# Kernel optimization log

Hardware: AMD Instinct MI355X
Metric: run time of the kernel (lower is better)

## Reference

```python
import jax, jax.numpy as jnp
import numpy as np


def setup_inputs() -> dict:
    key = jax.random.key(0)
    k1, k2, k3 = jax.random.split(key, 3)
    S, G, B, C, P = 3, 8, 2048, 512, 64
    node_feats = jax.random.normal(k1, (S, G * B, C), dtype=jnp.float32)
    weight = jax.random.normal(k2, (P, C), dtype=jnp.float32)
    smooth_factor = jax.random.normal(k3, (P,), dtype=jnp.float32)
    return {
        "node_feats": node_feats,
        "weight": weight,
        "smooth_factor": smooth_factor,
        "batch_size": B,
        "num_graphs": G,
    }


def reference(node_feats, weight, smooth_factor, batch_size, num_graphs):
    # node_feats: [S, N_scale, C] (scales stacked; torch version takes a list and cats)
    S, Ns, C = node_feats.shape
    P = weight.shape[0]
    x = node_feats.reshape(-1, C)                       # [N, C], N = S*Ns

    # RBF-style score: (2*c.x - |x|^2 - |c|^2), clamped at 0, scaled by beta
    cx = x @ weight.T                                   # [N, P]
    x_sq = jnp.sum(x * x, axis=1, keepdims=True)        # [N, 1]
    c_sq = jnp.sum(weight * weight, axis=1)[None, :]    # [1, P]
    beta = jax.nn.sigmoid(smooth_factor)                # [P]
    logits = jnp.minimum(2.0 * cx - x_sq - c_sq, 0.0) / beta[None, :]
    assign = jax.nn.softmax(logits, axis=1)             # [N, P]

    # Per-graph weighted sum (uniform batch_list), accumulated across scales:
    # out[g] = sum_{s,n in graph g} assign[s,g,n]^T feats[s,g,n]
    a = assign.reshape(S, num_graphs, batch_size, P)
    f = node_feats.reshape(S, num_graphs, batch_size, C)
    outputs = jnp.einsum('sgnp,sgnc->gpc', a, f)        # [G, P, C]
    return outputs, assign
```

## Files before the change

kernel.cpp:

```cpp
#include <hip/hip_runtime.h>
#include <math.h>

#define S_ 3
#define G_ 8
#define B_ 2048
#define C_ 512
#define P_ 64
#define N_ (S_ * G_ * B_)

typedef __attribute__((ext_vector_type(8))) short short8;
typedef __attribute__((ext_vector_type(4))) float f32x4;
typedef __attribute__((ext_vector_type(4))) unsigned int uint4v;
typedef __attribute__((ext_vector_type(2))) unsigned int uint2v;

__device__ __forceinline__ unsigned f2bf1(float f) {
    union { float f; unsigned u; } c; c.f = f;
    unsigned u = c.u;
    u += 0x7fffu + ((u >> 16) & 1u);
    return u >> 16;
}
__device__ __forceinline__ unsigned pk2(float a, float b) {
    return f2bf1(a) | (f2bf1(b) << 16);
}

__global__ void zero_kernel(float* __restrict__ out) {
    int i = blockIdx.x * blockDim.x + threadIdx.x;
    ((f32x4*)out)[i] = (f32x4){0.f, 0.f, 0.f, 0.f};
}

__global__ __launch_bounds__(64) void prep_kernel(
    const float* __restrict__ w, const float* __restrict__ sf,
    unsigned short* __restrict__ wb, float* __restrict__ csq,
    float* __restrict__ rbeta)
{
    const int p = blockIdx.x, l = threadIdx.x;
    const float* wr = w + (size_t)p * C_ + l * 8;
    f32x4 a = *(const f32x4*)wr;
    f32x4 b = *(const f32x4*)(wr + 4);
    float s = a[0]*a[0] + a[1]*a[1] + a[2]*a[2] + a[3]*a[3]
            + b[0]*b[0] + b[1]*b[1] + b[2]*b[2] + b[3]*b[3];
    uint4v pk;
    pk.x = pk2(a[0], a[1]); pk.y = pk2(a[2], a[3]);
    pk.z = pk2(b[0], b[1]); pk.w = pk2(b[2], b[3]);
    *(uint4v*)&wb[(size_t)p * C_ + l * 8] = pk;
#pragma unroll
    for (int off = 1; off < 64; off <<= 1) s += __shfl_xor(s, off, 64);
    if (l == 0) csq[p] = s;
    if (p == 0) rbeta[l] = 1.0f + expf(-sf[l]);
}

__global__ __launch_bounds__(256) void assign_v2(
    const float* __restrict__ x, const unsigned short* __restrict__ wb,
    const float* __restrict__ csq, const float* __restrict__ rbeta,
    float* __restrict__ assign, unsigned short* __restrict__ a_t)
{
    __shared__ float lg[64 * 68];

    const int t    = threadIdx.x;
    const int lane = t & 63;
    const int wv   = t >> 6;
    const int q    = lane >> 4;
    const int col  = lane & 15;
    const int n0   = blockIdx.x * 64;
    const int myrow = 16 * wv + col;

    const float* xr = x + (size_t)(n0 + myrow) * C_ + q * 8;

    float csqv[4], rbv[4];
#pragma unroll
    for (int t4 = 0; t4 < 4; ++t4) {
        csqv[t4] = csq[16 * t4 + col];
        rbv[t4]  = rbeta[16 * t4 + col];
    }

    f32x4 acc[4];
#pragma unroll
    for (int i = 0; i < 4; ++i) acc[i] = (f32x4){0.f, 0.f, 0.f, 0.f};
    float xsq = 0.f;

#pragma unroll
    for (int ks = 0; ks < 16; ++ks) {
        f32x4 a = *(const f32x4*)(xr + ks * 32);
        f32x4 b = *(const f32x4*)(xr + ks * 32 + 4);
        xsq += a[0]*a[0] + a[1]*a[1] + a[2]*a[2] + a[3]*a[3]
             + b[0]*b[0] + b[1]*b[1] + b[2]*b[2] + b[3]*b[3];
        union { uint4v u; short8 s; } cvt;
        cvt.u.x = pk2(a[0], a[1]); cvt.u.y = pk2(a[2], a[3]);
        cvt.u.z = pk2(b[0], b[1]); cvt.u.w = pk2(b[2], b[3]);
        short8 af = cvt.s;
#pragma unroll
        for (int t4 = 0; t4 < 4; ++t4) {
            short8 bf = *(const short8*)&wb[(size_t)(16 * t4 + col) * C_ + ks * 32 + q * 8];
            acc[t4] = __builtin_amdgcn_mfma_f32_16x16x32_bf16(af, bf, acc[t4], 0, 0, 0);
        }
    }

    xsq += __shfl_xor(xsq, 16, 64);
    xsq += __shfl_xor(xsq, 32, 64);
    float xsqr[4];
#pragma unroll
    for (int reg = 0; reg < 4; ++reg) xsqr[reg] = __shfl(xsq, 4 * q + reg, 64);

#pragma unroll
    for (int reg = 0; reg < 4; ++reg) {
        const int row = 16 * wv + 4 * q + reg;
        float vv[4], vmax = -3.4e38f;
#pragma unroll
        for (int t4 = 0; t4 < 4; ++t4) {
            float v = 2.0f * acc[t4][reg] - xsqr[reg] - csqv[t4];
            v = fminf(v, 0.0f) * rbv[t4];
            vv[t4] = v;
            vmax = fmaxf(vmax, v);
        }
#pragma unroll
        for (int off = 1; off < 16; off <<= 1)
            vmax = fmaxf(vmax, __shfl_xor(vmax, off, 64));
        float e[4], ss = 0.f;
#pragma unroll
        for (int t4 = 0; t4 < 4; ++t4) { e[t4] = __expf(vv[t4] - vmax); ss += e[t4]; }
#pragma unroll
        for (int off = 1; off < 16; off <<= 1)
            ss += __shfl_xor(ss, off, 64);
        const float inv = 1.0f / ss;
#pragma unroll
        for (int t4 = 0; t4 < 4; ++t4) {
            const float val = e[t4] * inv;
            assign[(size_t)(n0 + row) * P_ + 16 * t4 + col] = val;
            lg[row * 68 + 16 * t4 + col] = val;
        }
    }
    __syncthreads();

    const int p  = t >> 2;
    const int nq = t & 3;
    float v[16];
#pragma unroll
    for (int i = 0; i < 16; ++i) v[i] = lg[(nq * 16 + i) * 68 + p];
    uint4v d0, d1;
    d0.x = pk2(v[0], v[1]);  d0.y = pk2(v[2], v[3]);
    d0.z = pk2(v[4], v[5]);  d0.w = pk2(v[6], v[7]);
    d1.x = pk2(v[8], v[9]);  d1.y = pk2(v[10], v[11]);
    d1.z = pk2(v[12], v[13]); d1.w = pk2(v[14], v[15]);
    unsigned short* dst = a_t + (size_t)p * N_ + n0 + nq * 16;
    *(uint4v*)dst = d0;
    *(uint4v*)(dst + 8) = d1;
}

__global__ __launch_bounds__(256) void group_v3(
    const float* __restrict__ x, const unsigned short* __restrict__ a_t,
    float* __restrict__ out)
{
    __shared__ unsigned int fsu[64 * 36];

    const int t    = threadIdx.x;
    const int lane = t & 63;
    const int wv   = t >> 6;
    const int q    = lane >> 4;
    const int col  = lane & 15;
    const int g    = blockIdx.x;
    const int c0   = blockIdx.y * 64;
    const int kc   = blockIdx.z;
    const int sc   = kc >> 2;
    const int b0   = (kc & 3) * 512;
    const int srow = t >> 4;
    const int scol = t & 15;

    const size_t base = (size_t)sc * (G_ * B_) + (size_t)g * B_ + b0;
    const unsigned short* at_row = a_t + (size_t)(16 * wv + col) * N_ + base;

    f32x4 acc[4];
#pragma unroll
    for (int i = 0; i < 4; ++i) acc[i] = (f32x4){0.f, 0.f, 0.f, 0.f};

    for (int ch = 0; ch < 8; ++ch) {
        const int nb = ch * 64;
        const size_t rbase = (base + nb + srow * 4) * C_ + c0 + scol * 4;
        f32x4 m0 = *(const f32x4*)(x + rbase);
        f32x4 m1 = *(const f32x4*)(x + rbase + C_);
        f32x4 m2 = *(const f32x4*)(x + rbase + 2 * C_);
        f32x4 m3 = *(const f32x4*)(x + rbase + 3 * C_);
        const int sw_w = (scol & 6) << 3;
        const int nsw  = (srow * 4) ^ sw_w;
#pragma unroll
        for (int cc = 0; cc < 4; ++cc) {
            uint2v u;
            u.x = pk2(m0[cc], m1[cc]);
            u.y = pk2(m2[cc], m3[cc]);
            const int cl = scol * 4 + cc;
            *(uint2v*)&fsu[cl * 36 + (nsw >> 1)] = u;
        }
        __syncthreads();

#pragma unroll
        for (int stp = 0; stp < 2; ++stp) {
            const int kb = stp * 32 + q * 8;
            short8 af = *(const short8*)(at_row + nb + kb);
#pragma unroll
            for (int t4 = 0; t4 < 4; ++t4) {
                const int c  = 16 * t4 + col;
                const int sw = ((c >> 2) & 6) << 3;
                short8 bf = *(const short8*)&fsu[c * 36 + ((kb ^ sw) >> 1)];
                acc[t4] = __builtin_amdgcn_mfma_f32_16x16x32_bf16(af, bf, acc[t4], 0, 0, 0);
            }
        }
        __syncthreads();
    }

#pragma unroll
    for (int t4 = 0; t4 < 4; ++t4) {
#pragma unroll
        for (int reg = 0; reg < 4; ++reg) {
            const int p = 16 * wv + 4 * q + reg;
            const int c = c0 + 16 * t4 + col;
            atomicAdd(&out[(size_t)g * (P_ * C_) + (size_t)p * C_ + c], acc[t4][reg]);
        }
    }
}

extern "C" void kernel_launch(void* const* d_in, const int* in_sizes, int n_in,
                              void* d_out, int out_size, void* d_ws, size_t ws_size,
                              hipStream_t stream) {
    const float* x  = (const float*)d_in[0];
    const float* w  = (const float*)d_in[1];
    const float* sf = (const float*)d_in[2];

    float* out    = (float*)d_out;
    float* assign = out + (size_t)G_ * P_ * C_;

    unsigned short* wb    = (unsigned short*)d_ws;
    float*          csq   = (float*)((char*)d_ws + 65536);
    float*          rbeta = (float*)((char*)d_ws + 65792);
    unsigned short* a_t   = (unsigned short*)((char*)d_ws + 66048);

    zero_kernel<<<(G_ * P_ * C_) / (4 * 256), 256, 0, stream>>>(out);
    prep_kernel<<<P_, 64, 0, stream>>>(w, sf, wb, csq, rbeta);
    assign_v2<<<N_ / 64, 256, 0, stream>>>(x, wb, csq, rbeta, assign, a_t);
    dim3 gridB(G_, C_ / 64, 12);
    group_v3<<<gridB, 256, 0, stream>>>(x, a_t, out);
}
```

Measured before the change: 194.3 us.

## Stage x and weight tiles through LDS in assign and group GEMM kernels

The assign kernel now handles 128 rows per block and stages coalesced 64-column x chunks and bf16 weight chunks in shared memory. Each wave reuses the shared weight fragments across two M-tiles instead of re-reading them from global memory per lane. The group kernel now stages assignment rows in LDS as well and re-partitions the MFMA tiles so each wave owns a C slice. The intent is better coalescing and reuse of global loads, at the cost of more LDS traffic, extra barriers and fewer blocks in the assign kernel.

```diff
diff --git a/kernel.cpp b/kernel.cpp
--- a/kernel.cpp
+++ b/kernel.cpp
@@ -49,108 +49,158 @@
     if (p == 0) rbeta[l] = 1.0f + expf(-sf[l]);
 }
 
-__global__ __launch_bounds__(256) void assign_v2(
+#define XS_STR 68
+#define WS_STR 72
+__global__ __launch_bounds__(256, 3) void assign_gemm(
     const float* __restrict__ x, const unsigned short* __restrict__ wb,
     const float* __restrict__ csq, const float* __restrict__ rbeta,
     float* __restrict__ assign, unsigned short* __restrict__ a_t)
 {
-    __shared__ float lg[64 * 68];
+    __shared__ __align__(16) char smem[128 * XS_STR * 4 + 64 * WS_STR * 2];
+    float* xs = (float*)smem;
+    unsigned short* wsh = (unsigned short*)(smem + 128 * XS_STR * 4);
+    float* lg = (float*)smem;
 
     const int t    = threadIdx.x;
     const int lane = t & 63;
     const int wv   = t >> 6;
     const int q    = lane >> 4;
     const int col  = lane & 15;
-    const int n0   = blockIdx.x * 64;
-    const int myrow = 16 * wv + col;
-
-    const float* xr = x + (size_t)(n0 + myrow) * C_ + q * 8;
+    const int n0   = blockIdx.x * 128;
 
     float csqv[4], rbv[4];
 #pragma unroll
-    for (int t4 = 0; t4 < 4; ++t4) {
-        csqv[t4] = csq[16 * t4 + col];
-        rbv[t4]  = rbeta[16 * t4 + col];
-    }
-
-    f32x4 acc[4];
-#pragma unroll
-    for (int i = 0; i < 4; ++i) acc[i] = (f32x4){0.f, 0.f, 0.f, 0.f};
-    float xsq = 0.f;
-
-#pragma unroll
-    for (int ks = 0; ks < 16; ++ks) {
-        f32x4 a = *(const f32x4*)(xr + ks * 32);
-        f32x4 b = *(const f32x4*)(xr + ks * 32 + 4);
-        xsq += a[0]*a[0] + a[1]*a[1] + a[2]*a[2] + a[3]*a[3]
-             + b[0]*b[0] + b[1]*b[1] + b[2]*b[2] + b[3]*b[3];
-        union { uint4v u; short8 s; } cvt;
-        cvt.u.x = pk2(a[0], a[1]); cvt.u.y = pk2(a[2], a[3]);
-        cvt.u.z = pk2(b[0], b[1]); cvt.u.w = pk2(b[2], b[3]);
-        short8 af = cvt.s;
-#pragma unroll
-        for (int t4 = 0; t4 < 4; ++t4) {
-            short8 bf = *(const short8*)&wb[(size_t)(16 * t4 + col) * C_ + ks * 32 + q * 8];
-            acc[t4] = __builtin_amdgcn_mfma_f32_16x16x32_bf16(af, bf, acc[t4], 0, 0, 0);
-        }
-    }
-
-    xsq += __shfl_xor(xsq, 16, 64);
-    xsq += __shfl_xor(xsq, 32, 64);
-    float xsqr[4];
-#pragma unroll
-    for (int reg = 0; reg < 4; ++reg) xsqr[reg] = __shfl(xsq, 4 * q + reg, 64);
-
-#pragma unroll
-    for (int reg = 0; reg < 4; ++reg) {
-        const int row = 16 * wv + 4 * q + reg;
-        float vv[4], vmax = -3.4e38f;
-#pragma unroll
-        for (int t4 = 0; t4 < 4; ++t4) {
-            float v = 2.0f * acc[t4][reg] - xsqr[reg] - csqv[t4];
-            v = fminf(v, 0.0f) * rbv[t4];
-            vv[t4] = v;
-            vmax = fmaxf(vmax, v);
-        }
-#pragma unroll
-        for (int off = 1; off < 16; off <<= 1)
-            vmax = fmaxf(vmax, __shfl_xor(vmax, off, 64));
-        float e[4], ss = 0.f;
-#pragma unroll
-        for (int t4 = 0; t4 < 4; ++t4) { e[t4] = __expf(vv[t4] - vmax); ss += e[t4]; }
-#pragma unroll
-        for (int off = 1; off < 16; off <<= 1)
-            ss += __shfl_xor(ss, off, 64);
-        const float inv = 1.0f / ss;
-#pragma unroll
-        for (int t4 = 0; t4 < 4; ++t4) {
-            const float val = e[t4] * inv;
-            assign[(size_t)(n0 + row) * P_ + 16 * t4 + col] = val;
-            lg[row * 68 + 16 * t4 + col] = val;
+    for (int nt = 0; nt < 4; ++nt) {
+        csqv[nt] = csq[16 * nt + col];
+        rbv[nt]  = rbeta[16 * nt + col];
+    }
+
+    f32x4 acc[2][4];
+#pragma unroll
+    for (int mt = 0; mt < 2; ++mt)
+#pragma unroll
+        for (int nt = 0; nt < 4; ++nt) acc[mt][nt] = (f32x4){0.f, 0.f, 0.f, 0.f};
+    float xsq[2] = {0.f, 0.f};
+
+    const int srow = lane >> 4;
+    const int sseg = lane & 15;
+    const int wp   = lane >> 3;
+    const int wseg = lane & 7;
+
+    for (int ch = 0; ch < 8; ++ch) {
+        const int k0 = ch * 64;
+#pragma unroll
+        for (int i = 0; i < 8; ++i) {
+            const int row = wv * 32 + i * 4 + srow;
+            f32x4 v = *(const f32x4*)(x + (size_t)(n0 + row) * C_ + k0 + sseg * 4);
+            *(f32x4*)&xs[row * XS_STR + sseg * 4] = v;
+        }
+#pragma unroll
+        for (int i = 0; i < 2; ++i) {
+            const int p = wv * 16 + i * 8 + wp;
+            uint4v wv4 = *(const uint4v*)&wb[(size_t)p * C_ + k0 + wseg * 8];
+            *(uint4v*)&wsh[p * WS_STR + wseg * 8] = wv4;
+        }
+        __syncthreads();
+
+#pragma unroll
+        for (int s = 0; s < 2; ++s) {
+            const int koff = s * 32 + q * 8;
+            short8 bf[4];
+#pragma unroll
+            for (int nt = 0; nt < 4; ++nt)
+                bf[nt] = *(const short8*)&wsh[(16 * nt + col) * WS_STR + koff];
+#pragma unroll
+            for (int mt = 0; mt < 2; ++mt) {
+                const int row = wv * 32 + 16 * mt + col;
+                f32x4 f0 = *(const f32x4*)&xs[row * XS_STR + koff];
+                f32x4 f1 = *(const f32x4*)&xs[row * XS_STR + koff + 4];
+                xsq[mt] += f0.x*f0.x + f0.y*f0.y + f0.z*f0.z + f0.w*f0.w
+                         + f1.x*f1.x + f1.y*f1.y + f1.z*f1.z + f1.w*f1.w;
+                union { uint4v u; short8 s8; } cv;
+                cv.u.x = pk2(f0.x, f0.y); cv.u.y = pk2(f0.z, f0.w);
+                cv.u.z = pk2(f1.x, f1.y); cv.u.w = pk2(f1.z, f1.w);
+#pragma unroll
+                for (int nt = 0; nt < 4; ++nt)
+                    acc[mt][nt] = __builtin_amdgcn_mfma_f32_16x16x32_bf16(
+                        cv.s8, bf[nt], acc[mt][nt], 0, 0, 0);
+            }
+        }
+        __syncthreads();
+    }
+
+#pragma unroll
+    for (int mt = 0; mt < 2; ++mt) {
+        xsq[mt] += __shfl_xor(xsq[mt], 16, 64);
+        xsq[mt] += __shfl_xor(xsq[mt], 32, 64);
+    }
+    float xsqr[2][4];
+#pragma unroll
+    for (int mt = 0; mt < 2; ++mt)
+#pragma unroll
+        for (int reg = 0; reg < 4; ++reg)
+            xsqr[mt][reg] = __shfl(xsq[mt], 4 * q + reg, 64);
+
+#pragma unroll
+    for (int mt = 0; mt < 2; ++mt) {
+#pragma unroll
+        for (int reg = 0; reg < 4; ++reg) {
+            const int row = wv * 32 + 16 * mt + 4 * q + reg;
+            float vv[4], vmax = -3.4e38f;
+#pragma unroll
+            for (int nt = 0; nt < 4; ++nt) {
+                float v = 2.0f * acc[mt][nt][reg] - xsqr[mt][reg] - csqv[nt];
+                v = fminf(v, 0.0f) * rbv[nt];
+                vv[nt] = v;
+                vmax = fmaxf(vmax, v);
+            }
+#pragma unroll
+            for (int off = 1; off < 16; off <<= 1)
+                vmax = fmaxf(vmax, __shfl_xor(vmax, off, 64));
+            float e[4], ss = 0.f;
+#pragma unroll
+            for (int nt = 0; nt < 4; ++nt) { e[nt] = __expf(vv[nt] - vmax); ss += e[nt]; }
+#pragma unroll
+            for (int off = 1; off < 16; off <<= 1)
+                ss += __shfl_xor(ss, off, 64);
+            const float inv = 1.0f / ss;
+#pragma unroll
+            for (int nt = 0; nt < 4; ++nt) {
+                const float val = e[nt] * inv;
+                assign[(size_t)(n0 + row) * P_ + 16 * nt + col] = val;
+                lg[row * XS_STR + 16 * nt + col] = val;
+            }
         }
     }
     __syncthreads();
 
-    const int p  = t >> 2;
-    const int nq = t & 3;
-    float v[16];
-#pragma unroll
-    for (int i = 0; i < 16; ++i) v[i] = lg[(nq * 16 + i) * 68 + p];
+    const int p    = t & 63;
+    const int nbas = wv * 32;
+    float v[32];
+#pragma unroll
+    for (int i = 0; i < 32; ++i) v[i] = lg[(nbas + i) * XS_STR + p];
     uint4v d0, d1;
-    d0.x = pk2(v[0], v[1]);  d0.y = pk2(v[2], v[3]);
-    d0.z = pk2(v[4], v[5]);  d0.w = pk2(v[6], v[7]);
-    d1.x = pk2(v[8], v[9]);  d1.y = pk2(v[10], v[11]);
+    d0.x = pk2(v[0], v[1]);   d0.y = pk2(v[2], v[3]);
+    d0.z = pk2(v[4], v[5]);   d0.w = pk2(v[6], v[7]);
+    d1.x = pk2(v[8], v[9]);   d1.y = pk2(v[10], v[11]);
     d1.z = pk2(v[12], v[13]); d1.w = pk2(v[14], v[15]);
-    unsigned short* dst = a_t + (size_t)p * N_ + n0 + nq * 16;
+    unsigned short* dst = a_t + (size_t)p * N_ + n0 + nbas;
     *(uint4v*)dst = d0;
     *(uint4v*)(dst + 8) = d1;
-}
-
-__global__ __launch_bounds__(256) void group_v3(
+    d0.x = pk2(v[16], v[17]); d0.y = pk2(v[18], v[19]);
+    d0.z = pk2(v[20], v[21]); d0.w = pk2(v[22], v[23]);
+    d1.x = pk2(v[24], v[25]); d1.y = pk2(v[26], v[27]);
+    d1.z = pk2(v[28], v[29]); d1.w = pk2(v[30], v[31]);
+    *(uint4v*)(dst + 16) = d0;
+    *(uint4v*)(dst + 24) = d1;
+}
+
+__global__ __launch_bounds__(256, 3) void group_gemm(
     const float* __restrict__ x, const unsigned short* __restrict__ a_t,
     float* __restrict__ out)
 {
-    __shared__ unsigned int fsu[64 * 36];
+    __shared__ __align__(16) unsigned short ash[64 * WS_STR];
+    __shared__ __align__(16) unsigned short xts[64 * WS_STR];
 
     const int t    = threadIdx.x;
     const int lane = t & 63;
@@ -159,60 +209,63 @@
     const int col  = lane & 15;
     const int g    = blockIdx.x;
     const int c0   = blockIdx.y * 64;
-    const int kc   = blockIdx.z;
-    const int sc   = kc >> 2;
-    const int b0   = (kc & 3) * 512;
-    const int srow = t >> 4;
+    const int ks   = blockIdx.z;
+    const int sc   = ks >> 2;
+    const int b0   = (ks & 3) * 512;
+    const size_t base = (size_t)sc * (G_ * B_) + (size_t)g * B_ + b0;
+
+    f32x4 acc[4];
+#pragma unroll
+    for (int mt = 0; mt < 4; ++mt) acc[mt] = (f32x4){0.f, 0.f, 0.f, 0.f};
+
+    const int ap   = t >> 3;
+    const int aseg = t & 7;
+    const int r0   = (t >> 4) * 4;
     const int scol = t & 15;
-
-    const size_t base = (size_t)sc * (G_ * B_) + (size_t)g * B_ + b0;
-    const unsigned short* at_row = a_t + (size_t)(16 * wv + col) * N_ + base;
-
-    f32x4 acc[4];
-#pragma unroll
-    for (int i = 0; i < 4; ++i) acc[i] = (f32x4){0.f, 0.f, 0.f, 0.f};
 
     for (int ch = 0; ch < 8; ++ch) {
         const int nb = ch * 64;
-        const size_t rbase = (base + nb + srow * 4) * C_ + c0 + scol * 4;
-        f32x4 m0 = *(const f32x4*)(x + rbase);
-        f32x4 m1 = *(const f32x4*)(x + rbase + C_);
-        f32x4 m2 = *(const f32x4*)(x + rbase + 2 * C_);
-        f32x4 m3 = *(const f32x4*)(x + rbase + 3 * C_);
-        const int sw_w = (scol & 6) << 3;
-        const int nsw  = (srow * 4) ^ sw_w;
+#pragma unroll
+        for (int i = 0; i < 2; ++i) {
+            const int p = i * 32 + ap;
+            uint4v av = *(const uint4v*)&a_t[(size_t)p * N_ + base + nb + aseg * 8];
+            *(uint4v*)&ash[p * WS_STR + aseg * 8] = av;
+        }
+        const size_t rb = (base + nb + r0) * C_ + c0 + scol * 4;
+        f32x4 m0 = *(const f32x4*)(x + rb);
+        f32x4 m1 = *(const f32x4*)(x + rb + C_);
+        f32x4 m2 = *(const f32x4*)(x + rb + 2 * C_);
+        f32x4 m3 = *(const f32x4*)(x + rb + 3 * C_);
 #pragma unroll
         for (int cc = 0; cc < 4; ++cc) {
+            const int c = scol * 4 + cc;
             uint2v u;
             u.x = pk2(m0[cc], m1[cc]);
             u.y = pk2(m2[cc], m3[cc]);
-            const int cl = scol * 4 + cc;
-            *(uint2v*)&fsu[cl * 36 + (nsw >> 1)] = u;
-        }
-        __syncthreads();
-
-#pragma unroll
-        for (int stp = 0; stp < 2; ++stp) {
-            const int kb = stp * 32 + q * 8;
-            short8 af = *(const short8*)(at_row + nb + kb);
-#pragma unroll
-            for (int t4 = 0; t4 < 4; ++t4) {
-                const int c  = 16 * t4 + col;
-                const int sw = ((c >> 2) & 6) << 3;
-                short8 bf = *(const short8*)&fsu[c * 36 + ((kb ^ sw) >> 1)];
-                acc[t4] = __builtin_amdgcn_mfma_f32_16x16x32_bf16(af, bf, acc[t4], 0, 0, 0);
-            }
-        }
-        __syncthreads();
-    }
-
-#pragma unroll
-    for (int t4 = 0; t4 < 4; ++t4) {
+            *(uint2v*)&xts[c * WS_STR + r0] = u;
+        }
+        __syncthreads();
+
+#pragma unroll
+        for (int s = 0; s < 2; ++s) {
+            const int koff = s * 32 + q * 8;
+            short8 bfr = *(const short8*)&xts[(wv * 16 + col) * WS_STR + koff];
+#pragma unroll
+            for (int mt = 0; mt < 4; ++mt) {
+                short8 afr = *(const short8*)&ash[(16 * mt + col) * WS_STR + koff];
+                acc[mt] = __builtin_amdgcn_mfma_f32_16x16x32_bf16(afr, bfr, acc[mt], 0, 0, 0);
+            }
+        }
+        __syncthreads();
+    }
+
+#pragma unroll
+    for (int mt = 0; mt < 4; ++mt) {
 #pragma unroll
         for (int reg = 0; reg < 4; ++reg) {
-            const int p = 16 * wv + 4 * q + reg;
-            const int c = c0 + 16 * t4 + col;
-            atomicAdd(&out[(size_t)g * (P_ * C_) + (size_t)p * C_ + c], acc[t4][reg]);
+            const int p = 16 * mt + 4 * q + reg;
+            const int c = c0 + wv * 16 + col;
+            atomicAdd(&out[(size_t)g * (P_ * C_) + (size_t)p * C_ + c], acc[mt][reg]);
         }
     }
 }
@@ -234,7 +287,7 @@
 
     zero_kernel<<<(G_ * P_ * C_) / (4 * 256), 256, 0, stream>>>(out);
     prep_kernel<<<P_, 64, 0, stream>>>(w, sf, wb, csq, rbeta);
-    assign_v2<<<N_ / 64, 256, 0, stream>>>(x, wb, csq, rbeta, assign, a_t);
+    assign_gemm<<<N_ / 128, 256, 0, stream>>>(x, wb, csq, rbeta, assign, a_t);
     dim3 gridB(G_, C_ / 64, 12);
-    group_v3<<<gridB, 256, 0, stream>>>(x, a_t, out);
-}
+    group_gemm<<<gridB, 256, 0, stream>>>(x, a_t, out);
+}
```

After: 208.0 us. 1.07x slower.
